# Performance work log

Hardware: AMD Instinct MI355X
Metric: run time of the kernel (lower is better)

Reference implementation:

```python
import jax, jax.numpy as jnp
import numpy as np

NUM_HEADS = 16
EMBED_DIM = 128
SEQ_LEN = 1024
BATCH = 4


def setup_inputs() -> dict:
    key = jax.random.key(0)
    ks = jax.random.split(key, 5)
    x = jax.random.normal(ks[0], (BATCH, SEQ_LEN, EMBED_DIM), dtype=jnp.float32)
    scale = 0.02
    w_q = jax.random.normal(ks[1], (NUM_HEADS * EMBED_DIM, EMBED_DIM), dtype=jnp.float32) * scale
    w_k = jax.random.normal(ks[2], (NUM_HEADS * EMBED_DIM, EMBED_DIM), dtype=jnp.float32) * scale
    w_v = jax.random.normal(ks[3], (NUM_HEADS * EMBED_DIM, EMBED_DIM), dtype=jnp.float32) * scale
    w_o = jax.random.normal(ks[4], (EMBED_DIM, NUM_HEADS * EMBED_DIM), dtype=jnp.float32) * scale
    return {"x": x, "w_q": w_q, "w_k": w_k, "w_v": w_v, "w_o": w_o}


def _rope_tables(seq_len, embed_dim, dtype):
    half = embed_dim // 2
    # faithful to source: angles = 10000 ** (2*i / embed_dim)  (positive exponent)
    angles = jnp.power(jnp.asarray(10000.0, dtype), 2.0 * jnp.arange(half, dtype=dtype) / embed_dim)
    theta = jnp.arange(seq_len, dtype=dtype)[:, None] * angles[None, :]  # [S, half]
    return jnp.cos(theta), jnp.sin(theta)


def _apply_rope(t, cos, sin):
    # t: [B, S, H, E] viewed as complex pairs on last dim
    B, S, H, E = t.shape
    tr = t.reshape(B, S, H, E // 2, 2)
    a, b = tr[..., 0], tr[..., 1]
    c = cos[None, :, None, :]
    s = sin[None, :, None, :]
    out = jnp.stack([a * c - b * s, a * s + b * c], axis=-1)
    return out.reshape(B, S, H, E)


def reference(x, w_q, w_k, w_v, w_o):
    B, S, E = x.shape
    H = NUM_HEADS
    q = jnp.einsum('bse,fe->bsf', x, w_q).reshape(B, S, H, E)
    k = jnp.einsum('bse,fe->bsf', x, w_k).reshape(B, S, H, E)
    v = jnp.einsum('bse,fe->bsf', x, w_v).reshape(B, S, H, E)
    cos, sin = _rope_tables(S, E, x.dtype)
    q = _apply_rope(q, cos, sin)
    k = _apply_rope(k, cos, sin)
    att = jnp.einsum('bqhd,bkhd->bhqk', q, k) / jnp.sqrt(jnp.asarray(E, x.dtype))
    causal = jnp.tril(jnp.ones((S, S), dtype=bool))[None, None]
    att = jnp.where(causal, att, jnp.asarray(-jnp.inf, x.dtype))
    att = jax.nn.softmax(att, axis=-1)
    y = jnp.einsum('bhqk,bkhd->bqhd', att, v).reshape(B, S, H * E)
    return jnp.einsum('bsf,ef->bse', y, w_o)
```

## Files before the change

### kernel.cpp

```cpp
#include <hip/hip_runtime.h>

typedef unsigned short u16;
typedef unsigned int   u32;
typedef __attribute__((ext_vector_type(8))) short bf8_t;
typedef __attribute__((ext_vector_type(4))) float f4_t;

#define SEQ   1024
#define NH    16
#define DH    128
#define BATCH 4
#define MROWS 4096
#define FDIM  2048

__device__ __forceinline__ u16 f2bf(float f) {
  union { float f; u32 u; } v; v.f = f;
  u32 u = v.u;
  u += 0x7fffu + ((u >> 16) & 1u);
  return (u16)(u >> 16);
}
__device__ __forceinline__ float bf2f(u16 b) {
  union { u32 u; float f; } v; v.u = ((u32)b) << 16;
  return v.f;
}

__global__ __launch_bounds__(256) void to_bf16(
    const float* __restrict__ x,  const float* __restrict__ wq,
    const float* __restrict__ wk, const float* __restrict__ wv,
    const float* __restrict__ wo,
    u16* __restrict__ xb, u16* __restrict__ wqb, u16* __restrict__ wkb,
    u16* __restrict__ wvb, u16* __restrict__ wob) {
  int i = blockIdx.x * 256 + threadIdx.x;
  const float* s; u16* d; int o;
  if      (i <  65536) { s = x;  d = xb;  o = i; }
  else if (i <  98304) { s = wq; d = wqb; o = i - 65536; }
  else if (i < 131072) { s = wk; d = wkb; o = i - 98304; }
  else if (i < 163840) { s = wv; d = wvb; o = i - 131072; }
  else                 { s = wo; d = wob; o = i - 163840; }
  const f4_t* sp = reinterpret_cast<const f4_t*>(s + (size_t)o * 8);
  f4_t a = sp[0], b = sp[1];
  bf8_t pk;
#pragma unroll
  for (int j = 0; j < 4; ++j) { pk[j] = (short)f2bf(a[j]); pk[4 + j] = (short)f2bf(b[j]); }
  *reinterpret_cast<bf8_t*>(d + (size_t)o * 8) = pk;
}

__global__ __launch_bounds__(256) void rope_tables(float* __restrict__ cosT,
                                                   float* __restrict__ sinT) {
  int i = blockIdx.x * 256 + threadIdx.x;
  int s = i >> 6, p = i & 63;
  float ef = (float)(2 * p) / 128.0f;
  float angf = (float)pow(10000.0, (double)ef);
  float thf  = (float)s * angf;
  double th  = (double)thf;
  cosT[i] = (float)cos(th);
  sinT[i] = (float)sin(th);
}

__global__ __launch_bounds__(256) void qkv_rope(
    const u16* __restrict__ xb,
    const u16* __restrict__ wqb, const u16* __restrict__ wkb,
    const u16* __restrict__ wvb,
    const float* __restrict__ cosT, const float* __restrict__ sinT,
    u16* __restrict__ qo, u16* __restrict__ ko, u16* __restrict__ vo) {
  __shared__ __align__(16) u16 a_lds[64 * 128];
  __shared__ __align__(16) u16 b_lds[64 * 128];
  const int tid = threadIdx.x;
  const int mt = blockIdx.x;
  const int by = blockIdx.y;
  const int mat = by >> 5;
  const int nt  = by & 31;
  const u16* w = (mat == 0) ? wqb : ((mat == 1) ? wkb : wvb);
  const int m0 = mt * 64, n0 = nt * 64;

#pragma unroll
  for (int i = 0; i < 4; ++i) {
    int idx = tid + i * 256;
    int row = idx >> 4, e0 = (idx & 15) * 8;
    int hw = ((row << 7) | e0) ^ ((row & 7) << 3);
    bf8_t xa = *reinterpret_cast<const bf8_t*>(xb + (size_t)(m0 + row) * 128 + e0);
    *reinterpret_cast<bf8_t*>(&a_lds[hw]) = xa;
    bf8_t wa = *reinterpret_cast<const bf8_t*>(w + (size_t)(n0 + row) * 128 + e0);
    *reinterpret_cast<bf8_t*>(&b_lds[hw]) = wa;
  }
  __syncthreads();

  const int lane = tid & 63, wid = tid >> 6;
  const int wr = wid >> 1, wc = wid & 1;
  const int g = lane >> 4, c16 = lane & 15;
  f4_t acc[2][2];
#pragma unroll
  for (int a = 0; a < 2; ++a)
#pragma unroll
    for (int b = 0; b < 2; ++b) acc[a][b] = (f4_t)0.0f;

#pragma unroll
  for (int kc = 0; kc < 4; ++kc) {
    bf8_t af[2], bf_[2];
#pragma unroll
    for (int fr = 0; fr < 2; ++fr) {
      int row = wr * 32 + fr * 16 + c16;
      int hw = ((row << 7) | (kc * 32 + g * 8)) ^ ((row & 7) << 3);
      af[fr] = *reinterpret_cast<const bf8_t*>(&a_lds[hw]);
    }
#pragma unroll
    for (int fc = 0; fc < 2; ++fc) {
      int row = wc * 32 + fc * 16 + c16;
      int hw = ((row << 7) | (kc * 32 + g * 8)) ^ ((row & 7) << 3);
      bf_[fc] = *reinterpret_cast<const bf8_t*>(&b_lds[hw]);
    }
#pragma unroll
    for (int fr = 0; fr < 2; ++fr)
#pragma unroll
      for (int fc = 0; fc < 2; ++fc)
        acc[fr][fc] = __builtin_amdgcn_mfma_f32_16x16x32_bf16(af[fr], bf_[fc], acc[fr][fc], 0, 0, 0);
  }

  if (mat == 2) {
    __syncthreads();
#pragma unroll
    for (int fr = 0; fr < 2; ++fr)
#pragma unroll
      for (int fc = 0; fc < 2; ++fc)
#pragma unroll
        for (int j = 0; j < 4; ++j) {
          int fcol = wc * 32 + fc * 16 + c16;
          int m = wr * 32 + fr * 16 + g * 4 + j;
          a_lds[fcol * 72 + m] = f2bf(acc[fr][fc][j]);
        }
    __syncthreads();
    const int b = mt >> 4, sl0 = m0 & 1023;
    const int hq = nt >> 1, dvb = (nt & 1) * 64;
#pragma unroll
    for (int i = 0; i < 2; ++i) {
      int r = tid >> 2, c0 = ((tid & 3) * 2 + i) * 8;
      bf8_t v = *reinterpret_cast<const bf8_t*>(&a_lds[r * 72 + c0]);
      size_t adr = ((size_t)((b * 16 + hq) * 128 + dvb + r)) * 1024 + sl0 + c0;
      *reinterpret_cast<bf8_t*>(vo + adr) = v;
    }
    return;
  }

  u16* outp = (mat == 0) ? qo : ko;
#pragma unroll
  for (int fr = 0; fr < 2; ++fr) {
#pragma unroll
    for (int fc = 0; fc < 2; ++fc) {
      int fcol = n0 + wc * 32 + fc * 16 + c16;
      int h = fcol >> 7, d = fcol & 127, p = d >> 1;
#pragma unroll
      for (int j = 0; j < 4; ++j) {
        int m = m0 + wr * 32 + fr * 16 + g * 4 + j;
        int b = m >> 10, sl = m & 1023;
        float v = acc[fr][fc][j];
        float vx = __shfl_xor(v, 1);
        float cv = cosT[sl * 64 + p], sv = sinT[sl * 64 + p];
        if (!(lane & 1)) {
          float e_out = v * cv - vx * sv;
          float o_out = v * sv + vx * cv;
          u32 u = (u32)f2bf(e_out) | ((u32)f2bf(o_out) << 16);
          u32 elem = ((u32)((b * 16 + h) * 1024 + sl)) * 128 + (u32)d;
          reinterpret_cast<u32*>(outp)[elem >> 1] = u;
        }
      }
    }
  }
}

__device__ __forceinline__ void stage_kv(const u16* __restrict__ Kp,
                                         const u16* __restrict__ Vt, int t,
                                         int tid, u16* k_lds, u16* vT) {
#pragma unroll
  for (int i = 0; i < 4; ++i) {
    int n = tid >> 2, c0 = ((tid & 3) * 4 + i) * 8;
    bf8_t kv = *reinterpret_cast<const bf8_t*>(Kp + (size_t)(t * 64 + n) * 128 + c0);
    *reinterpret_cast<bf8_t*>(&k_lds[n * 128 + (c0 ^ ((n & 7) << 3))]) = kv;
    int dv = tid >> 1, c1 = ((tid & 1) * 4 + i) * 8;
    bf8_t vv = *reinterpret_cast<const bf8_t*>(Vt + (size_t)dv * 1024 + t * 64 + c1);
    *reinterpret_cast<bf8_t*>(&vT[dv * 72 + c1]) = vv;
  }
}

__global__ __launch_bounds__(256, 3) void attn(
    const u16* __restrict__ qw, const u16* __restrict__ kw,
    const u16* __restrict__ vtg, u16* __restrict__ yw) {
  __shared__ __align__(16) u16 k_lds[64 * 128];
  __shared__ __align__(16) u16 vT[144 * 72];
  __shared__ __align__(16) u16 p_lds[4][16 * 64];
  const int tid = threadIdx.x, lane = tid & 63, wid = tid >> 6;
  const int g = lane >> 4, c16 = lane & 15;
  const int bid = blockIdx.x;
  const int pp = 15 - (bid >> 6);
  const int bh = bid & 63;
  const int b = bh >> 4, h = bh & 15;
  const int qt = 2 * pp + (wid >> 1);
  const int T = pp + 1;
  const u16* Qp = qw + (size_t)bh * SEQ * DH;
  const u16* Kp = kw + (size_t)bh * SEQ * DH;
  const u16* Vt = vtg + (size_t)bh * DH * SEQ;
  const float kscale = 0.08838834764831845f * 1.4426950408889634f;
  const int qrow0 = qt * 32 + (wid & 1) * 16;
  const int moff = (wid >> 1) * 32 + (wid & 1) * 16;

  {
    int r = 128 + (tid >> 4), c0 = (tid & 15) * 4;
    u16 v = (r == 128) ? (u16)0x3F80 : (u16)0;
#pragma unroll
    for (int e = 0; e < 4; ++e) vT[r * 72 + c0 + e] = v;
  }

  bf8_t qf[4];
#pragma unroll
  for (int c = 0; c < 4; ++c)
    qf[c] = *reinterpret_cast<const bf8_t*>(Qp + (size_t)(qrow0 + c16) * 128 + c * 32 + g * 8);

  f4_t yacc[9];
#pragma unroll
  for (int f = 0; f < 9; ++f) yacc[f] = (f4_t)0.0f;
  float m_run[4];
#pragma unroll
  for (int j = 0; j < 4; ++j) m_run[j] = -3e38f;

  stage_kv(Kp, Vt, 0, tid, k_lds, vT);
  __syncthreads();

  for (int t = 0; t < T; ++t) {
    f4_t sf[4];
#pragma unroll
    for (int nf = 0; nf < 4; ++nf) sf[nf] = (f4_t)0.0f;
    __builtin_amdgcn_s_setprio(1);
#pragma unroll
    for (int nf = 0; nf < 4; ++nf) {
      int row = nf * 16 + c16;
#pragma unroll
      for (int kc = 0; kc < 4; ++kc) {
        int hw = ((row << 7) | (kc * 32 + g * 8)) ^ ((row & 7) << 3);
        bf8_t kf = *reinterpret_cast<const bf8_t*>(&k_lds[hw]);
        sf[nf] = __builtin_amdgcn_mfma_f32_16x16x32_bf16(qf[kc], kf, sf[nf], 0, 0, 0);
      }
    }
    __builtin_amdgcn_s_setprio(0);

    if (t == T - 1) {
#pragma unroll
      for (int nf = 0; nf < 4; ++nf) {
        int keyc = nf * 16 + c16;
#pragma unroll
        for (int j = 0; j < 4; ++j)
          if (keyc > moff + g * 4 + j) sf[nf][j] = -3e38f;
      }
    }

    int chk = 0;
#pragma unroll
    for (int j = 0; j < 4; ++j) {
      float lmx = fmaxf(fmaxf(sf[0][j], sf[1][j]), fmaxf(sf[2][j], sf[3][j]));
      chk |= (lmx > m_run[j] + 32.0f) ? 1 : 0;
    }
    if (__any(chk)) {
      float lm[4];
#pragma unroll
      for (int j = 0; j < 4; ++j) {
        lm[j] = fmaxf(fmaxf(sf[0][j], sf[1][j]), fmaxf(sf[2][j], sf[3][j]));
        lm[j] = fmaxf(lm[j], __shfl_xor(lm[j], 1));
        lm[j] = fmaxf(lm[j], __shfl_xor(lm[j], 2));
        lm[j] = fmaxf(lm[j], __shfl_xor(lm[j], 4));
        lm[j] = fmaxf(lm[j], __shfl_xor(lm[j], 8));
      }
#pragma unroll
      for (int j = 0; j < 4; ++j) {
        float mn = fmaxf(m_run[j], lm[j]);
        float alpha = exp2f((m_run[j] - mn) * kscale);
        m_run[j] = mn;
#pragma unroll
        for (int f = 0; f < 9; ++f) yacc[f][j] *= alpha;
      }
    }

#pragma unroll
    for (int nf = 0; nf < 4; ++nf) {
#pragma unroll
      for (int j = 0; j < 4; ++j) {
        float pv = exp2f((sf[nf][j] - m_run[j]) * kscale);
        int q = g * 4 + j, n = nf * 16 + c16;
        int hw = ((q << 6) | n) ^ ((q & 7) << 3);
        p_lds[wid][hw] = f2bf(pv);
      }
    }
    bf8_t pa[2];
#pragma unroll
    for (int cc = 0; cc < 2; ++cc) {
      int hw = ((c16 << 6) | (cc * 32 + g * 8)) ^ ((c16 & 7) << 3);
      pa[cc] = *reinterpret_cast<const bf8_t*>(&p_lds[wid][hw]);
    }

    __builtin_amdgcn_s_setprio(1);
#pragma unroll
    for (int f = 0; f < 9; ++f) {
#pragma unroll
      for (int cc = 0; cc < 2; ++cc) {
        bf8_t vf = *reinterpret_cast<const bf8_t*>(&vT[(f * 16 + c16) * 72 + cc * 32 + g * 8]);
        yacc[f] = __builtin_amdgcn_mfma_f32_16x16x32_bf16(pa[cc], vf, yacc[f], 0, 0, 0);
      }
    }
    __builtin_amdgcn_s_setprio(0);

    __syncthreads();
    if (t + 1 < T) {
      stage_kv(Kp, Vt, t + 1, tid, k_lds, vT);
      __syncthreads();
    }
  }

  float rl[4];
#pragma unroll
  for (int j = 0; j < 4; ++j) {
    float lv = __shfl(yacc[8][j], lane & 48);
    rl[j] = 1.0f / lv;
  }
#pragma unroll
  for (int f = 0; f < 8; ++f) {
#pragma unroll
    for (int j = 0; j < 4; ++j) {
      float yv = yacc[f][j] * rl[j];
      float yn = __shfl_xor(yv, 1);
      if (!(lane & 1)) {
        int s_ = qrow0 + g * 4 + j;
        int dv = f * 16 + c16;
        u32 u = (u32)f2bf(yv) | ((u32)f2bf(yn) << 16);
        u32 elem = ((u32)(b * 1024 + s_)) * 2048 + (u32)(h * 128 + dv);
        reinterpret_cast<u32*>(yw)[elem >> 1] = u;
      }
    }
  }
}

__global__ __launch_bounds__(256) void oproj(
    const u16* __restrict__ yw, const u16* __restrict__ wob,
    float* __restrict__ out) {
  __shared__ __align__(16) u16 a_lds[64 * 64];
  __shared__ __align__(16) u16 b_lds[64 * 64];
  const int tid = threadIdx.x, lane = tid & 63, wid = tid >> 6;
  const int g = lane >> 4, c16 = lane & 15;
  const int wr = wid >> 1, wc = wid & 1;
  const int m0 = blockIdx.x * 64, n0 = blockIdx.y * 64;
  const int z = blockIdx.z;
  f4_t acc[2][2];
#pragma unroll
  for (int a = 0; a < 2; ++a)
#pragma unroll
    for (int b = 0; b < 2; ++b) acc[a][b] = (f4_t)0.0f;

  for (int kt = z * 16; kt < z * 16 + 16; ++kt) {
    int kb = kt * 64;
#pragma unroll
    for (int i = 0; i < 2; ++i) {
      int idx = tid + i * 256;
      int row = idx >> 3, k0 = (idx & 7) * 8;
      int hw = ((row << 6) | k0) ^ ((row & 7) << 3);
      bf8_t av = *reinterpret_cast<const bf8_t*>(yw + (size_t)(m0 + row) * 2048 + kb + k0);
      *reinterpret_cast<bf8_t*>(&a_lds[hw]) = av;
      bf8_t bv = *reinterpret_cast<const bf8_t*>(wob + (size_t)(n0 + row) * 2048 + kb + k0);
      *reinterpret_cast<bf8_t*>(&b_lds[hw]) = bv;
    }
    __syncthreads();
#pragma unroll
    for (int c = 0; c < 2; ++c) {
      bf8_t af[2], bf_[2];
#pragma unroll
      for (int fr = 0; fr < 2; ++fr) {
        int row = wr * 32 + fr * 16 + c16;
        int hw = ((row << 6) | (c * 32 + g * 8)) ^ ((row & 7) << 3);
        af[fr] = *reinterpret_cast<const bf8_t*>(&a_lds[hw]);
      }
#pragma unroll
      for (int fc = 0; fc < 2; ++fc) {
        int row = wc * 32 + fc * 16 + c16;
        int hw = ((row << 6) | (c * 32 + g * 8)) ^ ((row & 7) << 3);
        bf_[fc] = *reinterpret_cast<const bf8_t*>(&b_lds[hw]);
      }
#pragma unroll
      for (int fr = 0; fr < 2; ++fr)
#pragma unroll
        for (int fc = 0; fc < 2; ++fc)
          acc[fr][fc] = __builtin_amdgcn_mfma_f32_16x16x32_bf16(af[fr], bf_[fc], acc[fr][fc], 0, 0, 0);
    }
    __syncthreads();
  }
#pragma unroll
  for (int fr = 0; fr < 2; ++fr)
#pragma unroll
    for (int fc = 0; fc < 2; ++fc)
#pragma unroll
      for (int j = 0; j < 4; ++j) {
        int m = m0 + wr * 32 + fr * 16 + g * 4 + j;
        int e = n0 + wc * 32 + fc * 16 + c16;
        atomicAdd(&out[(size_t)m * 128 + e], acc[fr][fc][j]);
      }
}

extern "C" void kernel_launch(void* const* d_in, const int* in_sizes, int n_in,
                              void* d_out, int out_size, void* d_ws, size_t ws_size,
                              hipStream_t stream) {
  const float* x  = (const float*)d_in[0];
  const float* wq = (const float*)d_in[1];
  const float* wk = (const float*)d_in[2];
  const float* wv = (const float*)d_in[3];
  const float* wo = (const float*)d_in[4];
  float* out = (float*)d_out;

  char* ws = (char*)d_ws;
  const size_t NEED = (512ull << 10) + 4ull * (16ull << 20) + (3ull << 20);
  if (ws_size < NEED) return;
  float* cosT = (float*)ws;
  float* sinT = cosT + 64 * 1024;
  u16* qws = (u16*)(ws + (512 << 10));
  u16* kws = qws + (8u << 20);
  u16* vws = kws + (8u << 20);
  u16* yws = vws + (8u << 20);
  u16* xb  = yws + (8u << 20);
  u16* wqb = xb  + (1u << 19);
  u16* wkb = wqb + (1u << 18);
  u16* wvb = wkb + (1u << 18);
  u16* wob = wvb + (1u << 18);

  hipMemsetAsync(d_out, 0, (size_t)out_size * sizeof(float), stream);
  to_bf16<<<768, 256, 0, stream>>>(x, wq, wk, wv, wo, xb, wqb, wkb, wvb, wob);
  rope_tables<<<256, 256, 0, stream>>>(cosT, sinT);
  qkv_rope<<<dim3(64, 96), 256, 0, stream>>>(xb, wqb, wkb, wvb, cosT, sinT, qws, kws, vws);
  attn<<<1024, 256, 0, stream>>>(qws, kws, vws, yws);
  oproj<<<dim3(64, 2, 2), 256, 0, stream>>>(yws, wob, out);
}
```

Baseline: 99.47 us.

## Rewrite attention with 32x32x16 MFMA, register-resident P, and 2-wave blocks

The attention kernel now uses 32x32x16 bf16 MFMAs, computing S transposed (K as the A operand) so each lane holds one query's scores. P is converted with packed bf16 conversion and rearranged across the two half-waves by lane shuffles instead of a round trip through LDS. The row sum is kept in a register instead of an extra all-ones V column. Blocks shrink to 128 threads covering 64 query rows, with a new block-to-tile schedule that interleaves heavy and light causal tiles. The aim is fewer LDS round trips and MFMA instructions per tile, at the cost of more registers, smaller blocks, and unpaired 2-byte output stores.

Measured after the change: 154.6 us. 55.4% more time.

```diff
diff --git a/kernel.cpp b/kernel.cpp
--- a/kernel.cpp
+++ b/kernel.cpp
@@ -4,6 +4,7 @@
 typedef unsigned int   u32;
 typedef __attribute__((ext_vector_type(8))) short bf8_t;
 typedef __attribute__((ext_vector_type(4))) float f4_t;
+typedef __attribute__((ext_vector_type(16))) float f16v;
 
 #define SEQ   1024
 #define NH    16
@@ -18,9 +19,11 @@
   u += 0x7fffu + ((u >> 16) & 1u);
   return (u16)(u >> 16);
 }
-__device__ __forceinline__ float bf2f(u16 b) {
-  union { u32 u; float f; } v; v.u = ((u32)b) << 16;
-  return v.f;
+__device__ __forceinline__ u32 cvtpk(float a, float b) {
+  u32 r; asm("v_cvt_pk_bf16_f32 %0, %1, %2" : "=v"(r) : "v"(a), "v"(b)); return r;
+}
+__device__ __forceinline__ bf8_t mk8(u32 a, u32 b, u32 c, u32 d) {
+  union { u32 u[4]; bf8_t v; } x; x.u[0] = a; x.u[1] = b; x.u[2] = c; x.u[3] = d; return x.v;
 }
 
 __global__ __launch_bounds__(256) void to_bf16(
@@ -166,171 +169,164 @@
   }
 }
 
-__device__ __forceinline__ void stage_kv(const u16* __restrict__ Kp,
-                                         const u16* __restrict__ Vt, int t,
-                                         int tid, u16* k_lds, u16* vT) {
-#pragma unroll
-  for (int i = 0; i < 4; ++i) {
-    int n = tid >> 2, c0 = ((tid & 3) * 4 + i) * 8;
-    bf8_t kv = *reinterpret_cast<const bf8_t*>(Kp + (size_t)(t * 64 + n) * 128 + c0);
-    *reinterpret_cast<bf8_t*>(&k_lds[n * 128 + (c0 ^ ((n & 7) << 3))]) = kv;
-    int dv = tid >> 1, c1 = ((tid & 1) * 4 + i) * 8;
-    bf8_t vv = *reinterpret_cast<const bf8_t*>(Vt + (size_t)dv * 1024 + t * 64 + c1);
-    *reinterpret_cast<bf8_t*>(&vT[dv * 72 + c1]) = vv;
-  }
-}
-
-__global__ __launch_bounds__(256, 3) void attn(
+__device__ __forceinline__ void stage_kv32(const u16* __restrict__ Kp,
+                                           const u16* __restrict__ Vt, int t,
+                                           int tid, u16* k_lds, u16* vT) {
+#pragma unroll
+  for (int i = 0; i < 8; ++i) {
+    int ck = i * 128 + tid;
+    int n = ck >> 4, c = (ck & 15) * 8;
+    bf8_t kv = *reinterpret_cast<const bf8_t*>(Kp + (size_t)(t * 64 + n) * 128 + c);
+    *reinterpret_cast<bf8_t*>(&k_lds[((n << 7) | c) ^ ((n & 7) << 3)]) = kv;
+    int dv = ck >> 3, cc = (ck & 7) * 8;
+    bf8_t vv = *reinterpret_cast<const bf8_t*>(Vt + (size_t)dv * 1024 + t * 64 + cc);
+    *reinterpret_cast<bf8_t*>(&vT[dv * 72 + cc]) = vv;
+  }
+}
+
+__global__ __launch_bounds__(128, 2) void attn(
     const u16* __restrict__ qw, const u16* __restrict__ kw,
     const u16* __restrict__ vtg, u16* __restrict__ yw) {
   __shared__ __align__(16) u16 k_lds[64 * 128];
-  __shared__ __align__(16) u16 vT[144 * 72];
-  __shared__ __align__(16) u16 p_lds[4][16 * 64];
+  __shared__ __align__(16) u16 vT[128 * 72];
   const int tid = threadIdx.x, lane = tid & 63, wid = tid >> 6;
-  const int g = lane >> 4, c16 = lane & 15;
+  const int q32 = lane & 31, hi = lane >> 5;
   const int bid = blockIdx.x;
-  const int pp = 15 - (bid >> 6);
-  const int bh = bid & 63;
+  const int b6 = bid & 63, s6 = (bid >> 6) & 3, rnd = bid >> 8;
+  const int bh = (b6 & 7) * 8 + (b6 >> 3);
+  int qt;
+  if      (rnd == 0) qt = 12 + s6;
+  else if (rnd == 1) qt = 11 - s6;
+  else if (rnd == 2) qt = 4 + s6;
+  else               qt = 3 - s6;
+  const int T = qt + 1;
   const int b = bh >> 4, h = bh & 15;
-  const int qt = 2 * pp + (wid >> 1);
-  const int T = pp + 1;
   const u16* Qp = qw + (size_t)bh * SEQ * DH;
   const u16* Kp = kw + (size_t)bh * SEQ * DH;
   const u16* Vt = vtg + (size_t)bh * DH * SEQ;
   const float kscale = 0.08838834764831845f * 1.4426950408889634f;
-  const int qrow0 = qt * 32 + (wid & 1) * 16;
-  const int moff = (wid >> 1) * 32 + (wid & 1) * 16;
-
-  {
-    int r = 128 + (tid >> 4), c0 = (tid & 15) * 4;
-    u16 v = (r == 128) ? (u16)0x3F80 : (u16)0;
-#pragma unroll
-    for (int e = 0; e < 4; ++e) vT[r * 72 + c0 + e] = v;
-  }
-
-  bf8_t qf[4];
-#pragma unroll
-  for (int c = 0; c < 4; ++c)
-    qf[c] = *reinterpret_cast<const bf8_t*>(Qp + (size_t)(qrow0 + c16) * 128 + c * 32 + g * 8);
-
-  f4_t yacc[9];
-#pragma unroll
-  for (int f = 0; f < 9; ++f) yacc[f] = (f4_t)0.0f;
-  float m_run[4];
-#pragma unroll
-  for (int j = 0; j < 4; ++j) m_run[j] = -3e38f;
-
-  stage_kv(Kp, Vt, 0, tid, k_lds, vT);
+  const int qrow0 = qt * 64 + wid * 32;
+
+  bf8_t qf[8];
+#pragma unroll
+  for (int kc = 0; kc < 8; ++kc)
+    qf[kc] = *reinterpret_cast<const bf8_t*>(Qp + (size_t)(qrow0 + q32) * 128 + kc * 16 + hi * 8);
+
+  f16v y0 = (f16v)0.0f, y1 = (f16v)0.0f, y2 = (f16v)0.0f, y3 = (f16v)0.0f;
+  float m_run = -3e38f, l_run = 0.0f;
+
+  stage_kv32(Kp, Vt, 0, tid, k_lds, vT);
   __syncthreads();
 
   for (int t = 0; t < T; ++t) {
-    f4_t sf[4];
-#pragma unroll
-    for (int nf = 0; nf < 4; ++nf) sf[nf] = (f4_t)0.0f;
+    f16v sf0 = (f16v)0.0f, sf1 = (f16v)0.0f;
     __builtin_amdgcn_s_setprio(1);
 #pragma unroll
-    for (int nf = 0; nf < 4; ++nf) {
-      int row = nf * 16 + c16;
-#pragma unroll
-      for (int kc = 0; kc < 4; ++kc) {
-        int hw = ((row << 7) | (kc * 32 + g * 8)) ^ ((row & 7) << 3);
-        bf8_t kf = *reinterpret_cast<const bf8_t*>(&k_lds[hw]);
-        sf[nf] = __builtin_amdgcn_mfma_f32_16x16x32_bf16(qf[kc], kf, sf[nf], 0, 0, 0);
-      }
+    for (int kc = 0; kc < 8; ++kc) {
+      int c = kc * 16 + hi * 8;
+      bf8_t k0 = *reinterpret_cast<const bf8_t*>(&k_lds[((q32 << 7) | c) ^ ((q32 & 7) << 3)]);
+      bf8_t k1 = *reinterpret_cast<const bf8_t*>(&k_lds[(((32 + q32) << 7) | c) ^ ((q32 & 7) << 3)]);
+      sf0 = __builtin_amdgcn_mfma_f32_32x32x16_bf16(k0, qf[kc], sf0, 0, 0, 0);
+      sf1 = __builtin_amdgcn_mfma_f32_32x32x16_bf16(k1, qf[kc], sf1, 0, 0, 0);
     }
     __builtin_amdgcn_s_setprio(0);
 
     if (t == T - 1) {
-#pragma unroll
-      for (int nf = 0; nf < 4; ++nf) {
-        int keyc = nf * 16 + c16;
-#pragma unroll
-        for (int j = 0; j < 4; ++j)
-          if (keyc > moff + g * 4 + j) sf[nf][j] = -3e38f;
-      }
-    }
-
-    int chk = 0;
-#pragma unroll
-    for (int j = 0; j < 4; ++j) {
-      float lmx = fmaxf(fmaxf(sf[0][j], sf[1][j]), fmaxf(sf[2][j], sf[3][j]));
-      chk |= (lmx > m_run[j] + 32.0f) ? 1 : 0;
-    }
-    if (__any(chk)) {
-      float lm[4];
-#pragma unroll
-      for (int j = 0; j < 4; ++j) {
-        lm[j] = fmaxf(fmaxf(sf[0][j], sf[1][j]), fmaxf(sf[2][j], sf[3][j]));
-        lm[j] = fmaxf(lm[j], __shfl_xor(lm[j], 1));
-        lm[j] = fmaxf(lm[j], __shfl_xor(lm[j], 2));
-        lm[j] = fmaxf(lm[j], __shfl_xor(lm[j], 4));
-        lm[j] = fmaxf(lm[j], __shfl_xor(lm[j], 8));
-      }
-#pragma unroll
-      for (int j = 0; j < 4; ++j) {
-        float mn = fmaxf(m_run[j], lm[j]);
-        float alpha = exp2f((m_run[j] - mn) * kscale);
-        m_run[j] = mn;
-#pragma unroll
-        for (int f = 0; f < 9; ++f) yacc[f][j] *= alpha;
-      }
-    }
-
-#pragma unroll
-    for (int nf = 0; nf < 4; ++nf) {
-#pragma unroll
-      for (int j = 0; j < 4; ++j) {
-        float pv = exp2f((sf[nf][j] - m_run[j]) * kscale);
-        int q = g * 4 + j, n = nf * 16 + c16;
-        int hw = ((q << 6) | n) ^ ((q & 7) << 3);
-        p_lds[wid][hw] = f2bf(pv);
-      }
-    }
-    bf8_t pa[2];
-#pragma unroll
-    for (int cc = 0; cc < 2; ++cc) {
-      int hw = ((c16 << 6) | (cc * 32 + g * 8)) ^ ((c16 & 7) << 3);
-      pa[cc] = *reinterpret_cast<const bf8_t*>(&p_lds[wid][hw]);
-    }
+      int ql = wid * 32 + q32;
+#pragma unroll
+      for (int r = 0; r < 16; ++r) {
+        int kl = (r & 3) + 8 * (r >> 2) + 4 * hi;
+        if (kl > ql) sf0[r] = -3e38f;
+        if (kl + 32 > ql) sf1[r] = -3e38f;
+      }
+    }
+
+    float mx = sf0[0];
+#pragma unroll
+    for (int r = 1; r < 16; ++r) mx = fmaxf(mx, sf0[r]);
+#pragma unroll
+    for (int r = 0; r < 16; ++r) mx = fmaxf(mx, sf1[r]);
+    mx = fmaxf(mx, __shfl_xor(mx, 32));
+    if (__any(mx > m_run + 8.0f)) {
+      float mn = fmaxf(m_run, mx);
+      float al = exp2f((m_run - mn) * kscale);
+      m_run = mn;
+      l_run *= al;
+#pragma unroll
+      for (int r = 0; r < 16; ++r) {
+        int qp = (r & 3) + 8 * (r >> 2) + 4 * hi;
+        float alr = __shfl(al, qp + (lane & 32));
+        y0[r] *= alr; y1[r] *= alr; y2[r] *= alr; y3[r] *= alr;
+      }
+    }
+
+    float pv0[16], pv1[16];
+#pragma unroll
+    for (int r = 0; r < 16; ++r) {
+      pv0[r] = exp2f((sf0[r] - m_run) * kscale);
+      pv1[r] = exp2f((sf1[r] - m_run) * kscale);
+    }
+    float a0 = 0, a1 = 0, a2 = 0, a3 = 0;
+#pragma unroll
+    for (int r = 0; r < 16; r += 4) {
+      a0 += pv0[r] + pv1[r];         a1 += pv0[r + 1] + pv1[r + 1];
+      a2 += pv0[r + 2] + pv1[r + 2]; a3 += pv0[r + 3] + pv1[r + 3];
+    }
+    float sm = (a0 + a1) + (a2 + a3);
+    sm += __shfl_xor(sm, 32);
+    l_run += sm;
+
+    u32 W0[8], W1[8];
+#pragma unroll
+    for (int j = 0; j < 8; ++j) {
+      W0[j] = cvtpk(pv0[2 * j], pv0[2 * j + 1]);
+      W1[j] = cvtpk(pv1[2 * j], pv1[2 * j + 1]);
+    }
+    u32 sA0 = hi ? W0[0] : W0[2], sA1 = hi ? W0[1] : W0[3];
+    u32 sA2 = hi ? W0[4] : W0[6], sA3 = hi ? W0[5] : W0[7];
+    u32 sB0 = hi ? W1[0] : W1[2], sB1 = hi ? W1[1] : W1[3];
+    u32 sB2 = hi ? W1[4] : W1[6], sB3 = hi ? W1[5] : W1[7];
+    u32 rA0 = (u32)__shfl_xor((int)sA0, 32), rA1 = (u32)__shfl_xor((int)sA1, 32);
+    u32 rA2 = (u32)__shfl_xor((int)sA2, 32), rA3 = (u32)__shfl_xor((int)sA3, 32);
+    u32 rB0 = (u32)__shfl_xor((int)sB0, 32), rB1 = (u32)__shfl_xor((int)sB1, 32);
+    u32 rB2 = (u32)__shfl_xor((int)sB2, 32), rB3 = (u32)__shfl_xor((int)sB3, 32);
+    bf8_t pa0 = mk8(hi ? rA0 : W0[0], hi ? rA1 : W0[1], hi ? W0[2] : rA0, hi ? W0[3] : rA1);
+    bf8_t pa1 = mk8(hi ? rA2 : W0[4], hi ? rA3 : W0[5], hi ? W0[6] : rA2, hi ? W0[7] : rA3);
+    bf8_t pa2 = mk8(hi ? rB0 : W1[0], hi ? rB1 : W1[1], hi ? W1[2] : rB0, hi ? W1[3] : rB1);
+    bf8_t pa3 = mk8(hi ? rB2 : W1[4], hi ? rB3 : W1[5], hi ? W1[6] : rB2, hi ? W1[7] : rB3);
 
     __builtin_amdgcn_s_setprio(1);
-#pragma unroll
-    for (int f = 0; f < 9; ++f) {
-#pragma unroll
-      for (int cc = 0; cc < 2; ++cc) {
-        bf8_t vf = *reinterpret_cast<const bf8_t*>(&vT[(f * 16 + c16) * 72 + cc * 32 + g * 8]);
-        yacc[f] = __builtin_amdgcn_mfma_f32_16x16x32_bf16(pa[cc], vf, yacc[f], 0, 0, 0);
-      }
-    }
+#define PVDV(YY, DVB)                                                          \
+    { int vb = ((DVB) * 32 + q32) * 72 + hi * 8;                               \
+      bf8_t v0 = *reinterpret_cast<const bf8_t*>(&vT[vb]);                     \
+      bf8_t v1 = *reinterpret_cast<const bf8_t*>(&vT[vb + 16]);                \
+      bf8_t v2 = *reinterpret_cast<const bf8_t*>(&vT[vb + 32]);                \
+      bf8_t v3 = *reinterpret_cast<const bf8_t*>(&vT[vb + 48]);                \
+      YY = __builtin_amdgcn_mfma_f32_32x32x16_bf16(pa0, v0, YY, 0, 0, 0);      \
+      YY = __builtin_amdgcn_mfma_f32_32x32x16_bf16(pa1, v1, YY, 0, 0, 0);      \
+      YY = __builtin_amdgcn_mfma_f32_32x32x16_bf16(pa2, v2, YY, 0, 0, 0);      \
+      YY = __builtin_amdgcn_mfma_f32_32x32x16_bf16(pa3, v3, YY, 0, 0, 0); }
+    PVDV(y0, 0) PVDV(y1, 1) PVDV(y2, 2) PVDV(y3, 3)
+#undef PVDV
     __builtin_amdgcn_s_setprio(0);
 
     __syncthreads();
     if (t + 1 < T) {
-      stage_kv(Kp, Vt, t + 1, tid, k_lds, vT);
+      stage_kv32(Kp, Vt, t + 1, tid, k_lds, vT);
       __syncthreads();
     }
   }
 
-  float rl[4];
-#pragma unroll
-  for (int j = 0; j < 4; ++j) {
-    float lv = __shfl(yacc[8][j], lane & 48);
-    rl[j] = 1.0f / lv;
-  }
-#pragma unroll
-  for (int f = 0; f < 8; ++f) {
-#pragma unroll
-    for (int j = 0; j < 4; ++j) {
-      float yv = yacc[f][j] * rl[j];
-      float yn = __shfl_xor(yv, 1);
-      if (!(lane & 1)) {
-        int s_ = qrow0 + g * 4 + j;
-        int dv = f * 16 + c16;
-        u32 u = (u32)f2bf(yv) | ((u32)f2bf(yn) << 16);
-        u32 elem = ((u32)(b * 1024 + s_)) * 2048 + (u32)(h * 128 + dv);
-        reinterpret_cast<u32*>(yw)[elem >> 1] = u;
-      }
-    }
+  float rl = 1.0f / l_run;
+#pragma unroll
+  for (int r = 0; r < 16; ++r) {
+    int qp = (r & 3) + 8 * (r >> 2) + 4 * hi;
+    float rlr = __shfl(rl, qp + (lane & 32));
+    size_t base = ((size_t)(b * 1024 + qrow0 + qp)) * 2048 + h * 128 + q32;
+    yw[base]      = f2bf(y0[r] * rlr);
+    yw[base + 32] = f2bf(y1[r] * rlr);
+    yw[base + 64] = f2bf(y2[r] * rlr);
+    yw[base + 96] = f2bf(y3[r] * rlr);
   }
 }
 
@@ -427,6 +423,6 @@
   to_bf16<<<768, 256, 0, stream>>>(x, wq, wk, wv, wo, xb, wqb, wkb, wvb, wob);
   rope_tables<<<256, 256, 0, stream>>>(cosT, sinT);
   qkv_rope<<<dim3(64, 96), 256, 0, stream>>>(xb, wqb, wkb, wvb, cosT, sinT, qws, kws, vws);
-  attn<<<1024, 256, 0, stream>>>(qws, kws, vws, yws);
+  attn<<<1024, 128, 0, stream>>>(qws, kws, vws, yws);
   oproj<<<dim3(64, 2, 2), 256, 0, stream>>>(yws, wob, out);
 }
```

## Compute softmax row sums with shuffles instead of ones-row MFMA; swizzle V LDS

Applied to the files above, without the earlier changes.

The softmax denominator was obtained by appending a row of ones to the V tile and running a ninth output MFMA fragment. It is now accumulated in registers from the exponentials with shuffle reductions. This removes one of nine PV MFMA fragments, shrinks the accumulator and V LDS tile (144x72 padded to 128x64 XOR-swizzled), and raises the occupancy hint from 3 to 4 blocks. The block-to-q-tile mapping is also reordered into a snake pattern to balance causal work across dispatch rounds. Row sums now come from fp32 probabilities rather than bf16-rounded ones, and the extra shuffles add ALU work.

Measured after the change: 113.1 us. 1.14x slower.

```diff
diff --git a/kernel.cpp b/kernel.cpp
--- a/kernel.cpp
+++ b/kernel.cpp
@@ -17,10 +17,6 @@
   u32 u = v.u;
   u += 0x7fffu + ((u >> 16) & 1u);
   return (u16)(u >> 16);
-}
-__device__ __forceinline__ float bf2f(u16 b) {
-  union { u32 u; float f; } v; v.u = ((u32)b) << 16;
-  return v.f;
 }
 
 __global__ __launch_bounds__(256) void to_bf16(
@@ -173,23 +169,28 @@
   for (int i = 0; i < 4; ++i) {
     int n = tid >> 2, c0 = ((tid & 3) * 4 + i) * 8;
     bf8_t kv = *reinterpret_cast<const bf8_t*>(Kp + (size_t)(t * 64 + n) * 128 + c0);
-    *reinterpret_cast<bf8_t*>(&k_lds[n * 128 + (c0 ^ ((n & 7) << 3))]) = kv;
+    *reinterpret_cast<bf8_t*>(&k_lds[(n << 7) | (c0 ^ ((n & 7) << 3))]) = kv;
     int dv = tid >> 1, c1 = ((tid & 1) * 4 + i) * 8;
     bf8_t vv = *reinterpret_cast<const bf8_t*>(Vt + (size_t)dv * 1024 + t * 64 + c1);
-    *reinterpret_cast<bf8_t*>(&vT[dv * 72 + c1]) = vv;
-  }
-}
-
-__global__ __launch_bounds__(256, 3) void attn(
+    *reinterpret_cast<bf8_t*>(&vT[(dv << 6) | (c1 ^ ((dv & 7) << 3))]) = vv;
+  }
+}
+
+__global__ __launch_bounds__(256, 4) void attn(
     const u16* __restrict__ qw, const u16* __restrict__ kw,
     const u16* __restrict__ vtg, u16* __restrict__ yw) {
   __shared__ __align__(16) u16 k_lds[64 * 128];
-  __shared__ __align__(16) u16 vT[144 * 72];
+  __shared__ __align__(16) u16 vT[128 * 64];
   __shared__ __align__(16) u16 p_lds[4][16 * 64];
   const int tid = threadIdx.x, lane = tid & 63, wid = tid >> 6;
   const int g = lane >> 4, c16 = lane & 15;
   const int bid = blockIdx.x;
-  const int pp = 15 - (bid >> 6);
+  const int s6 = (bid >> 6) & 3, rnd = bid >> 8;
+  int pp;
+  if      (rnd == 0) pp = 15 - s6;
+  else if (rnd == 1) pp = 8 + s6;
+  else if (rnd == 2) pp = 7 - s6;
+  else               pp = s6;
   const int bh = bid & 63;
   const int b = bh >> 4, h = bh & 15;
   const int qt = 2 * pp + (wid >> 1);
@@ -201,24 +202,17 @@
   const int qrow0 = qt * 32 + (wid & 1) * 16;
   const int moff = (wid >> 1) * 32 + (wid & 1) * 16;
 
-  {
-    int r = 128 + (tid >> 4), c0 = (tid & 15) * 4;
-    u16 v = (r == 128) ? (u16)0x3F80 : (u16)0;
-#pragma unroll
-    for (int e = 0; e < 4; ++e) vT[r * 72 + c0 + e] = v;
-  }
-
   bf8_t qf[4];
 #pragma unroll
   for (int c = 0; c < 4; ++c)
     qf[c] = *reinterpret_cast<const bf8_t*>(Qp + (size_t)(qrow0 + c16) * 128 + c * 32 + g * 8);
 
-  f4_t yacc[9];
-#pragma unroll
-  for (int f = 0; f < 9; ++f) yacc[f] = (f4_t)0.0f;
-  float m_run[4];
-#pragma unroll
-  for (int j = 0; j < 4; ++j) m_run[j] = -3e38f;
+  f4_t yacc[8];
+#pragma unroll
+  for (int f = 0; f < 8; ++f) yacc[f] = (f4_t)0.0f;
+  float m_run[4], l_run[4];
+#pragma unroll
+  for (int j = 0; j < 4; ++j) { m_run[j] = -3e38f; l_run[j] = 0.0f; }
 
   stage_kv(Kp, Vt, 0, tid, k_lds, vT);
   __syncthreads();
@@ -233,7 +227,7 @@
       int row = nf * 16 + c16;
 #pragma unroll
       for (int kc = 0; kc < 4; ++kc) {
-        int hw = ((row << 7) | (kc * 32 + g * 8)) ^ ((row & 7) << 3);
+        int hw = (row << 7) | ((kc * 32 + g * 8) ^ ((row & 7) << 3));
         bf8_t kf = *reinterpret_cast<const bf8_t*>(&k_lds[hw]);
         sf[nf] = __builtin_amdgcn_mfma_f32_16x16x32_bf16(qf[kc], kf, sf[nf], 0, 0, 0);
       }
@@ -271,21 +265,35 @@
         float mn = fmaxf(m_run[j], lm[j]);
         float alpha = exp2f((m_run[j] - mn) * kscale);
         m_run[j] = mn;
-#pragma unroll
-        for (int f = 0; f < 9; ++f) yacc[f][j] *= alpha;
-      }
-    }
-
+        l_run[j] *= alpha;
+#pragma unroll
+        for (int f = 0; f < 8; ++f) yacc[f][j] *= alpha;
+      }
+    }
+
+    float rs[4];
+#pragma unroll
+    for (int j = 0; j < 4; ++j) rs[j] = 0.0f;
 #pragma unroll
     for (int nf = 0; nf < 4; ++nf) {
 #pragma unroll
       for (int j = 0; j < 4; ++j) {
         float pv = exp2f((sf[nf][j] - m_run[j]) * kscale);
+        rs[j] += pv;
         int q = g * 4 + j, n = nf * 16 + c16;
         int hw = ((q << 6) | n) ^ ((q & 7) << 3);
         p_lds[wid][hw] = f2bf(pv);
       }
     }
+#pragma unroll
+    for (int j = 0; j < 4; ++j) {
+      rs[j] += __shfl_xor(rs[j], 1);
+      rs[j] += __shfl_xor(rs[j], 2);
+      rs[j] += __shfl_xor(rs[j], 4);
+      rs[j] += __shfl_xor(rs[j], 8);
+      l_run[j] += rs[j];
+    }
+
     bf8_t pa[2];
 #pragma unroll
     for (int cc = 0; cc < 2; ++cc) {
@@ -295,12 +303,13 @@
 
     __builtin_amdgcn_s_setprio(1);
 #pragma unroll
-    for (int f = 0; f < 9; ++f) {
-#pragma unroll
-      for (int cc = 0; cc < 2; ++cc) {
-        bf8_t vf = *reinterpret_cast<const bf8_t*>(&vT[(f * 16 + c16) * 72 + cc * 32 + g * 8]);
-        yacc[f] = __builtin_amdgcn_mfma_f32_16x16x32_bf16(pa[cc], vf, yacc[f], 0, 0, 0);
-      }
+    for (int f = 0; f < 8; ++f) {
+      int row = f * 16 + c16;
+      int sw = (row & 7) << 3;
+      bf8_t v0 = *reinterpret_cast<const bf8_t*>(&vT[(row << 6) | ((g * 8) ^ sw)]);
+      bf8_t v1 = *reinterpret_cast<const bf8_t*>(&vT[(row << 6) | ((32 + g * 8) ^ sw)]);
+      yacc[f] = __builtin_amdgcn_mfma_f32_16x16x32_bf16(pa[0], v0, yacc[f], 0, 0, 0);
+      yacc[f] = __builtin_amdgcn_mfma_f32_16x16x32_bf16(pa[1], v1, yacc[f], 0, 0, 0);
     }
     __builtin_amdgcn_s_setprio(0);
 
@@ -313,10 +322,7 @@
 
   float rl[4];
 #pragma unroll
-  for (int j = 0; j < 4; ++j) {
-    float lv = __shfl(yacc[8][j], lane & 48);
-    rl[j] = 1.0f / lv;
-  }
+  for (int j = 0; j < 4; ++j) rl[j] = 1.0f / l_run[j];
 #pragma unroll
   for (int f = 0; f < 8; ++f) {
 #pragma unroll
```
